# Optimization experiments

Hardware: AMD Instinct MI355X
Metric: run time of the kernel (lower is better)

The kernel has to match this reference:

```python
import jax, jax.numpy as jnp
import numpy as np

H, W = 480, 640
FLOW_SCALING = float(max(H, W))  # config default: max(resolution)
REGUL_WEIGHT = 0.001
MAX_TS = 1.0  # single association pass
EPS = 1e-9


def setup_inputs() -> dict:
    key = jax.random.key(0)
    k1, k2, k3, k4, k5 = jax.random.split(key, 5)
    B, N = 8, 131072
    # scale flow so warped displacements (flow * flow_scaling) are O(tens of px)
    flow = jax.random.normal(k1, (B, 2, H, W), jnp.float32) * 0.05
    ts = jax.random.uniform(k2, (B, N, 1), dtype=jnp.float32)
    ys = jax.random.randint(k3, (B, N), 0, H, dtype=jnp.int32)
    xs = jax.random.randint(k4, (B, N), 0, W, dtype=jnp.int32)
    pol = jax.random.randint(k5, (B, N), 0, 2, dtype=jnp.int32)  # 1 = positive event
    return {"flow": flow, "ts": ts, "ys": ys, "xs": xs, "pol": pol}


def _get_interpolation(ys, xs, ts0, fy, fx, tref):
    """Warp events to tref and build bilinear splat indices/weights.
    ys/xs: [B,N] int; ts0: [B,N] float; fy/fx: per-event flow [B,N].
    Returns idx [B,4N] int32 (flattened y*W+x) and weights [B,4N]."""
    dt = tref - ts0
    wy = ys.astype(jnp.float32) + dt * fy * FLOW_SCALING  # warped y [B,N]
    wx = xs.astype(jnp.float32) + dt * fx * FLOW_SCALING  # warped x [B,N]
    ty = jnp.floor(wy)
    by = ty + 1.0
    lx = jnp.floor(wx)
    rx = lx + 1.0
    # corner order: top-left, top-right, bottom-left, bottom-right -> [B,4N]
    iy = jnp.concatenate([ty, ty, by, by], axis=1)
    ix = jnp.concatenate([lx, rx, lx, rx], axis=1)
    wy4 = jnp.tile(wy, (1, 4))
    wx4 = jnp.tile(wx, (1, 4))
    w = jnp.maximum(0.0, 1.0 - jnp.abs(wy4 - iy)) * jnp.maximum(0.0, 1.0 - jnp.abs(wx4 - ix))
    inb = (iy >= 0) & (iy < H) & (ix >= 0) & (ix < W)
    iy = jnp.where(inb, iy, 0.0)
    ix = jnp.where(inb, ix, 0.0)
    w = w * inb.astype(w.dtype)
    idx = (iy * W + ix).astype(jnp.int32)
    return idx, w


def _splat(idx, w):
    """Scatter-add weights into per-pixel image. idx,w: [B,4N] -> [B,H*W]."""
    B = idx.shape[0]
    out = jnp.zeros((B, H * W), dtype=w.dtype)
    return out.at[jnp.arange(B)[:, None], idx].add(w)


def reference(flow, ts, ys, xs, pol):
    B, N = ys.shape
    # gather per-event flow (x channel 0, y channel 1) at original event pixels
    flat = ys * W + xs  # [B,N]
    flow_flat = flow.reshape(B, 2, H * W)
    bidx = jnp.arange(B)[:, None]
    fx = flow_flat[bidx, 0, flat]
    fy = flow_flat[bidx, 1, flat]

    ts0 = ts[..., 0]
    ts4 = jnp.tile(ts0, (1, 4))
    pos4 = jnp.tile(pol.astype(jnp.float32), (1, 4))
    neg4 = 1.0 - pos4

    def iwe_loss(tref, ts_w):
        idx, w = _get_interpolation(ys, xs, ts0, fy, fx, tref)
        iwe_pos = _splat(idx, w * pos4)
        iwe_neg = _splat(idx, w * neg4)
        iwe_pos_ts = _splat(idx, w * ts_w * pos4) / (iwe_pos + EPS) / MAX_TS
        iwe_neg_ts = _splat(idx, w * ts_w * neg4) / (iwe_neg + EPS) / MAX_TS
        l = jnp.sum(iwe_pos_ts ** 2, axis=1) + jnp.sum(iwe_neg_ts ** 2, axis=1)
        nz = jnp.sum(((iwe_pos + iwe_neg) > 0).astype(l.dtype), axis=1)
        return jnp.sum(l / nz)

    fw_loss = iwe_loss(MAX_TS, ts4)
    bw_loss = iwe_loss(0.0, MAX_TS - ts4)

    # flow smoothness (charbonnier over 4 spatial directions)
    fxm = flow[:, 0:1]
    fym = flow[:, 1:2]
    charb = lambda a, b: jnp.sqrt(a * a + b * b + 1e-6)
    dx = charb(fxm[..., :, :-1] - fxm[..., :, 1:], fym[..., :, :-1] - fym[..., :, 1:])
    dy = charb(fxm[..., :-1, :] - fxm[..., 1:, :], fym[..., :-1, :] - fym[..., 1:, :])
    dr = charb(fxm[..., :-1, :-1] - fxm[..., 1:, 1:], fym[..., :-1, :-1] - fym[..., 1:, 1:])
    ur = charb(fxm[..., 1:, :-1] - fxm[..., :-1, 1:], fym[..., 1:, :-1] - fym[..., :-1, 1:])
    smooth = (jnp.mean(dx) + jnp.mean(dy) + jnp.mean(dr) + jnp.mean(ur)) / 4.0

    return fw_loss + bw_loss + REGUL_WEIGHT * smooth
```

## Files before the change

### kernel.cpp

```cpp
#include <hip/hip_runtime.h>


constexpr int H = 480, W = 640, HW = H * W;
constexpr int B = 8, N = 131072;
constexpr float FLOW_SCALING = 640.0f;
constexpr float EPS = 1e-9f;

constexpr int TH = 48, TW = 64;
constexpr int TILES_Y = H / TH;
constexpr int TILES_X = W / TW;
constexpr int TILES = TILES_Y * TILES_X;
constexpr int NBINS = B * 2 * TILES;
constexpr int CAP = 4096;

constexpr float PSCALE = 262144.0f;
constexpr float PINV = 1.0f / 262144.0f;

constexpr int BND_BLK = 44;
constexpr int SM_BLK = 512;
constexpr int SC_BLOCKS = 1024;

constexpr int EDGE_PX = 224;

constexpr int BPX = TILES_Y * W + TILES_X * H;

constexpr size_t ACCL_OFF = 0;
constexpr size_t ACCN_OFF = ACCL_OFF + (size_t)16 * TILES * 8;
constexpr size_t BNDL_OFF = ACCN_OFF + (size_t)16 * TILES * 8;
constexpr size_t BNDN_OFF = BNDL_OFF + (size_t)16 * BND_BLK * 8;
constexpr size_t SMP_OFF  = BNDN_OFF + (size_t)16 * BND_BLK * 8;
constexpr size_t CUR_OFF  = SMP_OFF + (size_t)SM_BLK * 4 * 8;
constexpr size_t BNDE_OFF = CUR_OFF + (size_t)NBINS * 4;
constexpr size_t BNDE_BYTES = (size_t)NBINS * EDGE_PX * 2 * 8;
constexpr size_t ITEMS_OFF = BNDE_OFF + BNDE_BYTES;

__device__ inline double blk_reduce(double v, double* sm) {
    __syncthreads();
    #pragma unroll
    for (int o = 32; o > 0; o >>= 1) v += __shfl_down(v, o, 64);
    int lane = threadIdx.x & 63;
    int wid  = threadIdx.x >> 6;
    if (lane == 0) sm[wid] = v;
    __syncthreads();
    double r = 0.0;
    if (threadIdx.x == 0) {
        int nw = (int)(blockDim.x >> 6);
        for (int w2 = 0; w2 < nw; ++w2) r += sm[w2];
    }
    return r;
}

__device__ inline int bin_from_payload(unsigned long long v) {
    int t = (int)(v & 1);
    int fyi = (int)((unsigned)(v >> 40) >> 12) - 512;
    int fxi = (int)(((unsigned)(v >> 16) & 0xFFFFFFu) >> 12) - 512;
    int cy = min(max(fyi, 0), H - 1);
    int cx = min(max(fxi, 0), W - 1);
    return t * TILES + (cy / TH) * TILES_X + (cx >> 6);
}

__device__ inline float charb(float a, float b) {
    return sqrtf(a * a + b * b + 1e-6f);
}

__global__ __launch_bounds__(256) void scatter_smooth_kernel(
    const float* __restrict__ flow, const float* __restrict__ ts,
    const int* __restrict__ ys, const int* __restrict__ xs,
    const int* __restrict__ pol,
    unsigned long long* __restrict__ items, unsigned* __restrict__ cursors,
    double* __restrict__ smP) {
    __shared__ unsigned scount[200];
    __shared__ unsigned sbase[200];
    __shared__ unsigned scur[200];
    __shared__ double sm[8];
    int tid = threadIdx.x;

    if (blockIdx.x < SM_BLK) {
        int sb = blockIdx.x;
        double sdx = 0.0, sdy = 0.0, sdr = 0.0, sur = 0.0;
        int stride = SM_BLK * 256;
        for (int i = sb * 256 + tid; i < B * HW; i += stride) {
            int b = i / HW;
            int rem = i - b * HW;
            int y = rem / W;
            int x = rem - y * W;
            const float* fx = flow + (size_t)(b * 2 + 0) * HW;
            const float* fy = flow + (size_t)(b * 2 + 1) * HW;
            float f00 = fx[rem], g00 = fy[rem];
            bool xe = (x + 1) < W;
            bool ye = (y + 1) < H;
            if (xe) {
                float f01 = fx[rem + 1], g01 = fy[rem + 1];
                sdx += (double)charb(f00 - f01, g00 - g01);
                if (ye) {
                    float f10 = fx[rem + W], g10 = fy[rem + W];
                    float f11 = fx[rem + W + 1], g11 = fy[rem + W + 1];
                    sdy += (double)charb(f00 - f10, g00 - g10);
                    sdr += (double)charb(f00 - f11, g00 - g11);
                    sur += (double)charb(f10 - f01, g10 - g01);
                }
            } else if (ye) {
                float f10 = fx[rem + W], g10 = fy[rem + W];
                sdy += (double)charb(f00 - f10, g00 - g10);
            }
        }
        double tt;
        tt = blk_reduce(sdx, sm); if (tid == 0) smP[sb * 4 + 0] = tt;
        tt = blk_reduce(sdy, sm); if (tid == 0) smP[sb * 4 + 1] = tt;
        tt = blk_reduce(sdr, sm); if (tid == 0) smP[sb * 4 + 2] = tt;
        tt = blk_reduce(sur, sm); if (tid == 0) smP[sb * 4 + 3] = tt;
        return;
    }

    if (tid < 200) { scount[tid] = 0; scur[tid] = 0; }
    __syncthreads();

    int sc = blockIdx.x - SM_BLK;
    int b = sc & 7;
    int chunk = sc >> 3;
    int e0 = b * N + chunk * 1024;
    const float* fb = flow + (size_t)b * 2 * HW;

    int y4[4], x4[4], p4[4];
    float t4[4];
    #pragma unroll
    for (int k = 0; k < 4; ++k) {
        int e = e0 + k * 256 + tid;
        y4[k] = ys[e];
        x4[k] = xs[e];
        p4[k] = pol[e];
        t4[k] = ts[e];
    }
    float fx4[4], fy4[4];
    #pragma unroll
    for (int k = 0; k < 4; ++k) {
        int flat = y4[k] * W + x4[k];
        fx4[k] = fb[flat];
        fy4[k] = fb[HW + flat];
    }

    unsigned long long pay[8];
    #pragma unroll
    for (int k = 0; k < 4; ++k) {
        float t0 = t4[k];
        #pragma unroll
        for (int t = 0; t < 2; ++t) {
            float dt = (t == 0 ? 1.0f : 0.0f) - t0;
            float sw = (t == 0) ? t0 : 1.0f - t0;
            float wy = (float)y4[k] + dt * fy4[k] * FLOW_SCALING;
            float wx = (float)x4[k] + dt * fx4[k] * FLOW_SCALING;
            unsigned long long v = ~0ull;
            if (wy >= -1.0f && wy < (float)H && wx >= -1.0f && wx < (float)W) {
                unsigned uy = __float2uint_rn((wy + 512.0f) * 4096.0f);
                unsigned ux = __float2uint_rn((wx + 512.0f) * 4096.0f);
                unsigned usw = __float2uint_rn(sw * 16383.0f);
                v = ((unsigned long long)uy << 40) |
                    ((unsigned long long)ux << 16) |
                    ((unsigned long long)usw << 2) |
                    ((unsigned long long)(p4[k] != 0) << 1) |
                    (unsigned long long)t;
                atomicAdd(&scount[bin_from_payload(v)], 1u);
            }
            pay[k * 2 + t] = v;
        }
    }
    __syncthreads();
    if (tid < 200) {
        unsigned c = scount[tid];
        sbase[tid] = c ? atomicAdd(&cursors[b * 200 + tid], c) : 0u;
    }
    __syncthreads();
    #pragma unroll
    for (int i = 0; i < 8; ++i) {
        unsigned long long v = pay[i];
        if (v == ~0ull) continue;
        int binl = bin_from_payload(v);
        unsigned idx = sbase[binl] + atomicAdd(&scur[binl], 1u);
        if (idx < (unsigned)CAP)
            items[(size_t)(b * 200 + binl) * CAP + idx] = v;
    }
}

__global__ __launch_bounds__(256) void accum_kernel(
    const unsigned long long* __restrict__ items,
    const unsigned* __restrict__ cursors,
    unsigned long long* __restrict__ bndE,
    double* __restrict__ accL, double* __restrict__ accN) {
    constexpr int TPX = (TH + 1) * (TW + 1);
    __shared__ unsigned long long sacc[2 * TPX];
    __shared__ double sm[8];
    int tid = threadIdx.x;
    for (int i = tid; i < 2 * TPX; i += 256) sacc[i] = 0ull;
    __syncthreads();

    int bin = blockIdx.x;
    int b = bin / 200;
    int loc = bin - b * 200;
    int t = loc / TILES;
    int tile = loc - t * TILES;
    int y0 = (tile / TILES_X) * TH;
    int x0 = (tile % TILES_X) * TW;
    int cnt = (int)min(cursors[bin], (unsigned)CAP);
    const unsigned long long* bi = items + (size_t)bin * CAP;

    for (int i = tid; i < cnt; i += 256) {
        unsigned long long v = bi[i];
        unsigned uy = (unsigned)(v >> 40);
        unsigned ux = (unsigned)(v >> 16) & 0xFFFFFFu;
        float wy = (float)uy * (1.0f / 4096.0f) - 512.0f;
        float wx = (float)ux * (1.0f / 4096.0f) - 512.0f;
        int fyi = (int)(uy >> 12) - 512;
        int fxi = (int)(ux >> 12) - 512;
        float sw = (float)((unsigned)(v >> 2) & 0x3FFFu) * (1.0f / 16383.0f);
        int f = ((v >> 1) & 1) ? 0 : 1;
        #pragma unroll
        for (int dy = 0; dy < 2; ++dy) {
            int ry = fyi + dy, ly = ry - y0;
            if (ry < 0 || ry >= H || ly < 0 || ly > TH) continue;
            float wfy = 1.0f - fabsf(wy - (float)ry);
            #pragma unroll
            for (int dx = 0; dx < 2; ++dx) {
                int rx = fxi + dx, lx = rx - x0;
                if (rx < 0 || rx >= W || lx < 0 || lx > TW) continue;
                float wgt = wfy * (1.0f - fabsf(wx - (float)rx));
                int px = ly * (TW + 1) + lx;
                unsigned w18 = __float2uint_rn(wgt * PSCALE);
                unsigned s18 = __float2uint_rn(wgt * sw * PSCALE);
                atomicAdd(&sacc[f * TPX + px],
                          ((unsigned long long)w18 << 32) | s18);
            }
        }
    }
    __syncthreads();

    double l = 0.0, nz = 0.0;
    unsigned long long* eb = bndE + (size_t)bin * EDGE_PX * 2;
    for (int p = tid; p < TPX; p += 256) {
        int ly = p / (TW + 1), lx = p - ly * (TW + 1);
        unsigned long long vp = sacc[p];
        unsigned long long vn = sacc[TPX + p];
        int slot = -1;
        if (ly == 0)           slot = lx;
        else if (ly == TH)     slot = 65 + lx;
        else if (lx == 0)      slot = 130 + (ly - 1);
        else if (lx == TW)     slot = 177 + (ly - 1);
        if (slot >= 0) {
            eb[(size_t)slot * 2]     = vp;
            eb[(size_t)slot * 2 + 1] = vn;
        } else {
            float fwp = (float)(unsigned)(vp >> 32) * PINV;
            float fsp = (float)(unsigned)vp * PINV;
            float fwn = (float)(unsigned)(vn >> 32) * PINV;
            float fsn = (float)(unsigned)vn * PINV;
            float a = fsp / (fwp + EPS);
            float c = fsn / (fwn + EPS);
            l += (double)(a * a + c * c);
            if ((vp | vn) >> 32) nz += 1.0;
        }
    }
    double lt = blk_reduce(l, sm);
    double nt = blk_reduce(nz, sm);
    if (tid == 0) {
        int j = b * 2 + t;
        accL[j * TILES + tile] = lt;
        accN[j * TILES + tile] = nt;
    }
}

__global__ __launch_bounds__(256) void bound_kernel(
    const unsigned long long* __restrict__ bndE,
    double* __restrict__ bndL, double* __restrict__ bndN) {
    __shared__ double sm[8];
    int j = blockIdx.y;
    int b = j >> 1, t = j & 1;
    const unsigned long long* jb =
        bndE + (size_t)(b * 200 + t * 100) * EDGE_PX * 2;

    double l = 0.0, nz = 0.0;
    for (int p = blockIdx.x * blockDim.x + threadIdx.x; p < BPX;
         p += gridDim.x * blockDim.x) {
        unsigned long long vp = 0ull, vn = 0ull;
        if (p < TILES_Y * W) {
            int k = p / W, x = p - k * W;
            int m = x >> 6, lx = x & 63;
            const unsigned long long* e;
            e = jb + ((size_t)(k * TILES_X + m) * EDGE_PX + lx) * 2;
            vp += e[0]; vn += e[1];
            if (k > 0) {
                e = jb + ((size_t)((k - 1) * TILES_X + m) * EDGE_PX + 65 + lx) * 2;
                vp += e[0]; vn += e[1];
            }
            if (lx == 0 && m > 0) {
                e = jb + ((size_t)(k * TILES_X + m - 1) * EDGE_PX + 64) * 2;
                vp += e[0]; vn += e[1];
                if (k > 0) {
                    e = jb + ((size_t)((k - 1) * TILES_X + m - 1) * EDGE_PX + 129) * 2;
                    vp += e[0]; vn += e[1];
                }
            }
        } else {
            int q = p - TILES_Y * W;
            int m = q / H, y = q - m * H;
            int r = y / TH, ly = y - r * TH;
            if (ly != 0) {
                const unsigned long long* e;
                e = jb + ((size_t)(r * TILES_X + m) * EDGE_PX + 130 + ly - 1) * 2;
                vp += e[0]; vn += e[1];
                if (m > 0) {
                    e = jb + ((size_t)(r * TILES_X + m - 1) * EDGE_PX + 177 + ly - 1) * 2;
                    vp += e[0]; vn += e[1];
                }
            }
        }
        unsigned wp = (unsigned)(vp >> 32), sp = (unsigned)vp;
        unsigned wn = (unsigned)(vn >> 32), sn = (unsigned)vn;
        float a = ((float)sp * PINV) / ((float)wp * PINV + EPS);
        float c = ((float)sn * PINV) / ((float)wn * PINV + EPS);
        l += (double)(a * a + c * c);
        if (wp | wn) nz += 1.0;
    }
    double lt = blk_reduce(l, sm);
    double nt = blk_reduce(nz, sm);
    if (threadIdx.x == 0) {
        bndL[j * BND_BLK + blockIdx.x] = lt;
        bndN[j * BND_BLK + blockIdx.x] = nt;
    }
}

__global__ __launch_bounds__(256) void final_kernel(
    const double* __restrict__ accL, const double* __restrict__ accN,
    const double* __restrict__ bndL, const double* __restrict__ bndN,
    const double* __restrict__ smP, float* __restrict__ out) {
    __shared__ double sj[16];
    __shared__ double sm[8];
    int tid = threadIdx.x;
    int j = tid >> 4, s = tid & 15;
    double l = 0.0, nz = 0.0;
    for (int i = s; i < TILES; i += 16) {
        l += accL[j * TILES + i];
        nz += accN[j * TILES + i];
    }
    for (int i = s; i < BND_BLK; i += 16) {
        l += bndL[j * BND_BLK + i];
        nz += bndN[j * BND_BLK + i];
    }
    #pragma unroll
    for (int o = 8; o > 0; o >>= 1) {
        l += __shfl_down(l, o, 16);
        nz += __shfl_down(nz, o, 16);
    }
    if (s == 0) sj[j] = l / nz;

    double c[4] = {0.0, 0.0, 0.0, 0.0};
    for (int i = tid; i < SM_BLK; i += 256) {
        #pragma unroll
        for (int k = 0; k < 4; ++k) c[k] += smP[i * 4 + k];
    }
    double s0 = blk_reduce(c[0], sm);
    double s1 = blk_reduce(c[1], sm);
    double s2 = blk_reduce(c[2], sm);
    double s3 = blk_reduce(c[3], sm);
    __syncthreads();
    if (tid == 0) {
        double loss = 0.0;
        for (int q = 0; q < 16; ++q) loss += sj[q];
        double ndx = (double)B * H * (W - 1);
        double ndy = (double)B * (H - 1) * W;
        double ndd = (double)B * (H - 1) * (W - 1);
        double smooth = (s0 / ndx + s1 / ndy + s2 / ndd + s3 / ndd) * 0.25;
        out[0] = (float)(loss + 0.001 * smooth);
    }
}

extern "C" void kernel_launch(void* const* d_in, const int* in_sizes, int n_in,
                              void* d_out, int out_size, void* d_ws, size_t ws_size,
                              hipStream_t stream) {
    const float* flow = (const float*)d_in[0];
    const float* ts   = (const float*)d_in[1];
    const int*   ys   = (const int*)d_in[2];
    const int*   xs   = (const int*)d_in[3];
    const int*   pol  = (const int*)d_in[4];
    float* out = (float*)d_out;

    char* ws = (char*)d_ws;
    double* accL = (double*)(ws + ACCL_OFF);
    double* accN = (double*)(ws + ACCN_OFF);
    double* bndL = (double*)(ws + BNDL_OFF);
    double* bndN = (double*)(ws + BNDN_OFF);
    double* smP  = (double*)(ws + SMP_OFF);
    unsigned* cursors = (unsigned*)(ws + CUR_OFF);
    unsigned long long* bndE = (unsigned long long*)(ws + BNDE_OFF);
    unsigned long long* items = (unsigned long long*)(ws + ITEMS_OFF);

    hipMemsetAsync(cursors, 0, (size_t)NBINS * 4, stream);
    scatter_smooth_kernel<<<SM_BLK + SC_BLOCKS, 256, 0, stream>>>(
        flow, ts, ys, xs, pol, items, cursors, smP);
    accum_kernel<<<NBINS, 256, 0, stream>>>(items, cursors, bndE, accL, accN);
    bound_kernel<<<dim3(BND_BLK, 16), 256, 0, stream>>>(bndE, bndL, bndN);
    final_kernel<<<1, 256, 0, stream>>>(accL, accN, bndL, bndN, smP, out);
}
```

Baseline: 150.0 us.

## Shrink binning tiles to 32x64, vectorize event loads, simplify loss math

Tile height drops from 48 to 32 rows. That gives more bins (300 per batch), so the accumulation kernel runs more, smaller blocks and each block holds a smaller shared-memory accumulator, at the cost of more boundary pixels. Per-event input loads become int4/float4 vector loads, and each event's bin index is cached in a register instead of being decoded again from the payload. The per-pixel loss now accumulates in float and int instead of double, and the scale factor is folded into EPS to remove multiplies. This slightly changes rounding, and the 32-row tiles need per-tile capacity (CAP 3072) to hold.

```diff
diff --git a/kernel.cpp b/kernel.cpp
--- a/kernel.cpp
+++ b/kernel.cpp
@@ -6,21 +6,21 @@
 constexpr float FLOW_SCALING = 640.0f;
 constexpr float EPS = 1e-9f;
 
-constexpr int TH = 48, TW = 64;
+constexpr int TH = 32, TW = 64;
 constexpr int TILES_Y = H / TH;
 constexpr int TILES_X = W / TW;
 constexpr int TILES = TILES_Y * TILES_X;
 constexpr int NBINS = B * 2 * TILES;
-constexpr int CAP = 4096;
+constexpr int CAP = 3072;
 
 constexpr float PSCALE = 262144.0f;
-constexpr float PINV = 1.0f / 262144.0f;
-
-constexpr int BND_BLK = 44;
+constexpr float EPS_S = PSCALE * EPS;
+
+constexpr int BND_BLK = 56;
 constexpr int SM_BLK = 512;
 constexpr int SC_BLOCKS = 1024;
 
-constexpr int EDGE_PX = 224;
+constexpr int EDGE_PX = 2 * (TW + 1) + 2 * (TH - 1);
 
 constexpr int BPX = TILES_Y * W + TILES_X * H;
 
@@ -56,7 +56,7 @@
     int fxi = (int)(((unsigned)(v >> 16) & 0xFFFFFFu) >> 12) - 512;
     int cy = min(max(fyi, 0), H - 1);
     int cx = min(max(fxi, 0), W - 1);
-    return t * TILES + (cy / TH) * TILES_X + (cx >> 6);
+    return t * TILES + (cy >> 5) * TILES_X + (cx >> 6);
 }
 
 __device__ inline float charb(float a, float b) {
@@ -69,9 +69,9 @@
     const int* __restrict__ pol,
     unsigned long long* __restrict__ items, unsigned* __restrict__ cursors,
     double* __restrict__ smP) {
-    __shared__ unsigned scount[200];
-    __shared__ unsigned sbase[200];
-    __shared__ unsigned scur[200];
+    __shared__ unsigned scount[2 * TILES];
+    __shared__ unsigned sbase[2 * TILES];
+    __shared__ unsigned scur[2 * TILES];
     __shared__ double sm[8];
     int tid = threadIdx.x;
 
@@ -112,25 +112,24 @@
         return;
     }
 
-    if (tid < 200) { scount[tid] = 0; scur[tid] = 0; }
+    for (int i = tid; i < 2 * TILES; i += 256) { scount[i] = 0; scur[i] = 0; }
     __syncthreads();
 
     int sc = blockIdx.x - SM_BLK;
     int b = sc & 7;
     int chunk = sc >> 3;
-    int e0 = b * N + chunk * 1024;
+    int eb0 = b * N + chunk * 1024;
     const float* fb = flow + (size_t)b * 2 * HW;
 
-    int y4[4], x4[4], p4[4];
-    float t4[4];
-    #pragma unroll
-    for (int k = 0; k < 4; ++k) {
-        int e = e0 + k * 256 + tid;
-        y4[k] = ys[e];
-        x4[k] = xs[e];
-        p4[k] = pol[e];
-        t4[k] = ts[e];
-    }
+    int4   yv = ((const int4*)(ys + eb0))[tid];
+    int4   xv = ((const int4*)(xs + eb0))[tid];
+    int4   pv = ((const int4*)(pol + eb0))[tid];
+    float4 tv = ((const float4*)(ts + eb0))[tid];
+    int y4[4] = {yv.x, yv.y, yv.z, yv.w};
+    int x4[4] = {xv.x, xv.y, xv.z, xv.w};
+    int p4[4] = {pv.x, pv.y, pv.z, pv.w};
+    float t4[4] = {tv.x, tv.y, tv.z, tv.w};
+
     float fx4[4], fy4[4];
     #pragma unroll
     for (int k = 0; k < 4; ++k) {
@@ -140,6 +139,7 @@
     }
 
     unsigned long long pay[8];
+    int bin8[8];
     #pragma unroll
     for (int k = 0; k < 4; ++k) {
         float t0 = t4[k];
@@ -150,6 +150,7 @@
             float wy = (float)y4[k] + dt * fy4[k] * FLOW_SCALING;
             float wx = (float)x4[k] + dt * fx4[k] * FLOW_SCALING;
             unsigned long long v = ~0ull;
+            int binl = -1;
             if (wy >= -1.0f && wy < (float)H && wx >= -1.0f && wx < (float)W) {
                 unsigned uy = __float2uint_rn((wy + 512.0f) * 4096.0f);
                 unsigned ux = __float2uint_rn((wx + 512.0f) * 4096.0f);
@@ -159,25 +160,26 @@
                     ((unsigned long long)usw << 2) |
                     ((unsigned long long)(p4[k] != 0) << 1) |
                     (unsigned long long)t;
-                atomicAdd(&scount[bin_from_payload(v)], 1u);
+                binl = bin_from_payload(v);
+                atomicAdd(&scount[binl], 1u);
             }
             pay[k * 2 + t] = v;
+            bin8[k * 2 + t] = binl;
         }
     }
     __syncthreads();
-    if (tid < 200) {
-        unsigned c = scount[tid];
-        sbase[tid] = c ? atomicAdd(&cursors[b * 200 + tid], c) : 0u;
+    for (int i = tid; i < 2 * TILES; i += 256) {
+        unsigned c = scount[i];
+        sbase[i] = c ? atomicAdd(&cursors[b * 2 * TILES + i], c) : 0u;
     }
     __syncthreads();
     #pragma unroll
     for (int i = 0; i < 8; ++i) {
-        unsigned long long v = pay[i];
-        if (v == ~0ull) continue;
-        int binl = bin_from_payload(v);
+        int binl = bin8[i];
+        if (binl < 0) continue;
         unsigned idx = sbase[binl] + atomicAdd(&scur[binl], 1u);
         if (idx < (unsigned)CAP)
-            items[(size_t)(b * 200 + binl) * CAP + idx] = v;
+            items[(size_t)(b * 2 * TILES + binl) * CAP + idx] = pay[i];
     }
 }
 
@@ -194,8 +196,8 @@
     __syncthreads();
 
     int bin = blockIdx.x;
-    int b = bin / 200;
-    int loc = bin - b * 200;
+    int b = bin / (2 * TILES);
+    int loc = bin - b * (2 * TILES);
     int t = loc / TILES;
     int tile = loc - t * TILES;
     int y0 = (tile / TILES_X) * TH;
@@ -233,7 +235,8 @@
     }
     __syncthreads();
 
-    double l = 0.0, nz = 0.0;
+    float lf = 0.0f;
+    int nzi = 0;
     unsigned long long* eb = bndE + (size_t)bin * EDGE_PX * 2;
     for (int p = tid; p < TPX; p += 256) {
         int ly = p / (TW + 1), lx = p - ly * (TW + 1);
@@ -241,25 +244,21 @@
         unsigned long long vn = sacc[TPX + p];
         int slot = -1;
         if (ly == 0)           slot = lx;
-        else if (ly == TH)     slot = 65 + lx;
-        else if (lx == 0)      slot = 130 + (ly - 1);
-        else if (lx == TW)     slot = 177 + (ly - 1);
+        else if (ly == TH)     slot = (TW + 1) + lx;
+        else if (lx == 0)      slot = 2 * (TW + 1) + (ly - 1);
+        else if (lx == TW)     slot = 2 * (TW + 1) + (TH - 1) + (ly - 1);
         if (slot >= 0) {
             eb[(size_t)slot * 2]     = vp;
             eb[(size_t)slot * 2 + 1] = vn;
         } else {
-            float fwp = (float)(unsigned)(vp >> 32) * PINV;
-            float fsp = (float)(unsigned)vp * PINV;
-            float fwn = (float)(unsigned)(vn >> 32) * PINV;
-            float fsn = (float)(unsigned)vn * PINV;
-            float a = fsp / (fwp + EPS);
-            float c = fsn / (fwn + EPS);
-            l += (double)(a * a + c * c);
-            if ((vp | vn) >> 32) nz += 1.0;
+            float a = (float)(unsigned)vp / ((float)(unsigned)(vp >> 32) + EPS_S);
+            float c = (float)(unsigned)vn / ((float)(unsigned)(vn >> 32) + EPS_S);
+            lf += a * a + c * c;
+            nzi += ((vp | vn) >> 32) != 0ull;
         }
     }
-    double lt = blk_reduce(l, sm);
-    double nt = blk_reduce(nz, sm);
+    double lt = blk_reduce((double)lf, sm);
+    double nt = blk_reduce((double)nzi, sm);
     if (tid == 0) {
         int j = b * 2 + t;
         accL[j * TILES + tile] = lt;
@@ -274,9 +273,10 @@
     int j = blockIdx.y;
     int b = j >> 1, t = j & 1;
     const unsigned long long* jb =
-        bndE + (size_t)(b * 200 + t * 100) * EDGE_PX * 2;
-
-    double l = 0.0, nz = 0.0;
+        bndE + (size_t)(b * 2 * TILES + t * TILES) * EDGE_PX * 2;
+
+    float lf = 0.0f;
+    int nzi = 0;
     for (int p = blockIdx.x * blockDim.x + threadIdx.x; p < BPX;
          p += gridDim.x * blockDim.x) {
         unsigned long long vp = 0ull, vn = 0ull;
@@ -287,14 +287,14 @@
             e = jb + ((size_t)(k * TILES_X + m) * EDGE_PX + lx) * 2;
             vp += e[0]; vn += e[1];
             if (k > 0) {
-                e = jb + ((size_t)((k - 1) * TILES_X + m) * EDGE_PX + 65 + lx) * 2;
+                e = jb + ((size_t)((k - 1) * TILES_X + m) * EDGE_PX + (TW + 1) + lx) * 2;
                 vp += e[0]; vn += e[1];
             }
             if (lx == 0 && m > 0) {
-                e = jb + ((size_t)(k * TILES_X + m - 1) * EDGE_PX + 64) * 2;
+                e = jb + ((size_t)(k * TILES_X + m - 1) * EDGE_PX + TW) * 2;
                 vp += e[0]; vn += e[1];
                 if (k > 0) {
-                    e = jb + ((size_t)((k - 1) * TILES_X + m - 1) * EDGE_PX + 129) * 2;
+                    e = jb + ((size_t)((k - 1) * TILES_X + m - 1) * EDGE_PX + 2 * TW + 1) * 2;
                     vp += e[0]; vn += e[1];
                 }
             }
@@ -304,23 +304,22 @@
             int r = y / TH, ly = y - r * TH;
             if (ly != 0) {
                 const unsigned long long* e;
-                e = jb + ((size_t)(r * TILES_X + m) * EDGE_PX + 130 + ly - 1) * 2;
+                e = jb + ((size_t)(r * TILES_X + m) * EDGE_PX + 2 * (TW + 1) + ly - 1) * 2;
                 vp += e[0]; vn += e[1];
                 if (m > 0) {
-                    e = jb + ((size_t)(r * TILES_X + m - 1) * EDGE_PX + 177 + ly - 1) * 2;
+                    e = jb + ((size_t)(r * TILES_X + m - 1) * EDGE_PX
+                              + 2 * (TW + 1) + (TH - 1) + ly - 1) * 2;
                     vp += e[0]; vn += e[1];
                 }
             }
         }
-        unsigned wp = (unsigned)(vp >> 32), sp = (unsigned)vp;
-        unsigned wn = (unsigned)(vn >> 32), sn = (unsigned)vn;
-        float a = ((float)sp * PINV) / ((float)wp * PINV + EPS);
-        float c = ((float)sn * PINV) / ((float)wn * PINV + EPS);
-        l += (double)(a * a + c * c);
-        if (wp | wn) nz += 1.0;
-    }
-    double lt = blk_reduce(l, sm);
-    double nt = blk_reduce(nz, sm);
+        float a = (float)(unsigned)vp / ((float)(unsigned)(vp >> 32) + EPS_S);
+        float c = (float)(unsigned)vn / ((float)(unsigned)(vn >> 32) + EPS_S);
+        lf += a * a + c * c;
+        nzi += ((vp | vn) >> 32) != 0ull;
+    }
+    double lt = blk_reduce((double)lf, sm);
+    double nt = blk_reduce((double)nzi, sm);
     if (threadIdx.x == 0) {
         bndL[j * BND_BLK + blockIdx.x] = lt;
         bndN[j * BND_BLK + blockIdx.x] = nt;
```

Result: faster. 145.7 us (-2.9%).
